# Kernel optimization log

Measured on AMD Instinct MI355X. Metric: run time of the kernel, lower is better.

## Reference

```python
import jax, jax.numpy as jnp
import numpy as np

B, L, V, D = 8, 2048, 1024, 512  # batch, seq (max_len), vocab_size (input feat), embedding_dim

def setup_inputs() -> dict:
    key = jax.random.key(0)
    kx, kq, kk, kv = jax.random.split(key, 4)
    scale = 1.0 / np.sqrt(V)
    return {
        "x": jax.random.normal(kx, (B, L, V), dtype=jnp.float32),
        "Wq": jax.random.uniform(kq, (D, V), dtype=jnp.float32, minval=-scale, maxval=scale),
        "Wk": jax.random.uniform(kk, (D, V), dtype=jnp.float32, minval=-scale, maxval=scale),
        "Wv": jax.random.uniform(kv, (D, V), dtype=jnp.float32, minval=-scale, maxval=scale),
    }

def reference(x, Wq, Wk, Wv):
    # nn.Linear without bias: y = x @ W.T
    q = jnp.einsum('blv,dv->bld', x, Wq)
    k = jnp.einsum('blv,dv->bld', x, Wk)
    v = jnp.einsum('blv,dv->bld', x, Wv)
    scores = jnp.einsum('bqd,bkd->bqk', q, k) / jnp.sqrt(jnp.float32(D))
    attn = jax.nn.softmax(scores, axis=2)
    return jnp.einsum('bqk,bkd->bqd', attn, v)
```

## Files before the change

### kernel.cpp

```cpp
#include <hip/hip_runtime.h>
#include <cstdint>
#include <cstddef>


typedef __attribute__((ext_vector_type(8))) __bf16 bf16x8;
typedef __attribute__((ext_vector_type(4))) float f32x4;
typedef __attribute__((ext_vector_type(4))) unsigned short ushort4v;
typedef __attribute__((ext_vector_type(4))) unsigned int uint4v;

__device__ __forceinline__ unsigned short f2bf(float f) {
  unsigned u = __float_as_uint(f);
  return (unsigned short)((u + 0x7fffu + ((u >> 16) & 1u)) >> 16);
}

__device__ __forceinline__ void async_load16(const unsigned short* g, unsigned short* l) {
  __builtin_amdgcn_global_load_lds(
      (__attribute__((address_space(1))) void*)(g),
      (__attribute__((address_space(3))) void*)(l), 16, 0, 0);
}

__global__ __launch_bounds__(256) void cvt_f32_bf16(const float* __restrict__ src,
                                                    unsigned short* __restrict__ dst) {
  int i = (blockIdx.x * 256 + threadIdx.x) * 4;
  float4 v = *(const float4*)(src + i);
  ushort4v o;
  o.x = f2bf(v.x); o.y = f2bf(v.y); o.z = f2bf(v.z); o.w = f2bf(v.w);
  *(ushort4v*)(dst + i) = o;
}

__global__ __launch_bounds__(256) void cvt_w3(const float* __restrict__ a,
                                              const float* __restrict__ b,
                                              const float* __restrict__ c,
                                              unsigned short* __restrict__ dst) {
  int bx = blockIdx.x;
  const float* src = (bx < 512) ? a : (bx < 1024) ? b : c;
  int seg = (bx < 512) ? 0 : (bx < 1024) ? 1 : 2;
  int i = ((bx & 511) * 256 + threadIdx.x) * 4;
  float4 v = *(const float4*)(src + i);
  ushort4v o;
  o.x = f2bf(v.x); o.y = f2bf(v.y); o.z = f2bf(v.z); o.w = f2bf(v.w);
  *(ushort4v*)(dst + seg * 524288 + i) = o;
}

__device__ __forceinline__ void stage_tile(
    const unsigned short* __restrict__ A, const unsigned short* __restrict__ B,
    size_t ldA, size_t ldB, unsigned short* buf, int tid, int k0) {
  int r = tid >> 3, c = tid & 7;
  int cs = (c ^ (r & 7)) * 8;
  #pragma unroll
  for (int p = 0; p < 4; ++p)
    async_load16(&A[(size_t)(p * 64 + r) * ldA + k0 + cs], &buf[(p * 512 + tid) * 8]);
  unsigned short* bb = buf + 16384;
  #pragma unroll
  for (int p = 0; p < 2; ++p)
    async_load16(&B[(size_t)(p * 64 + r) * ldB + k0 + cs], &bb[(p * 512 + tid) * 8]);
}

template <int NT, bool RSUM>
__device__ __forceinline__ void gemm_core(
    const unsigned short* __restrict__ A, const unsigned short* __restrict__ B,
    size_t ldA, size_t ldB, unsigned short* smem, int tid,
    f32x4 (&acc)[4][4], float (&rsum)[4]) {
  const int lane = tid & 63;
  const int wid = tid >> 6;
  const int wm = wid & 3, wn = wid >> 2;
  const int cl = lane & 15, g = lane >> 4;

  stage_tile(A, B, ldA, ldB, smem + 0 * 24576, tid, 0);
  stage_tile(A, B, ldA, ldB, smem + 1 * 24576, tid, 64);

  int cur = 0;
  for (int t = 0; t < NT; ++t) {
    if (t == NT - 1) asm volatile("s_waitcnt vmcnt(0)" ::: "memory");
    else             asm volatile("s_waitcnt vmcnt(6)" ::: "memory");
    __builtin_amdgcn_s_barrier();
    if (t + 2 < NT) {
      int nb = cur + 2; if (nb >= 3) nb -= 3;
      stage_tile(A, B, ldA, ldB, smem + nb * 24576, tid, (t + 2) * 64);
    }
    const unsigned short* sA = smem + cur * 24576;
    const unsigned short* sB = sA + 16384;

    bf16x8 aF[4][2], bF[4][2];
    #pragma unroll
    for (int mt = 0; mt < 4; ++mt)
      #pragma unroll
      for (int kh = 0; kh < 2; ++kh) {
        int row = wm * 64 + mt * 16 + cl;
        int ch = (kh * 4 + g) ^ (row & 7);
        aF[mt][kh] = *(const bf16x8*)&sA[(row * 8 + ch) * 8];
      }
    #pragma unroll
    for (int nt = 0; nt < 4; ++nt)
      #pragma unroll
      for (int kh = 0; kh < 2; ++kh) {
        int row = wn * 64 + nt * 16 + cl;
        int ch = (kh * 4 + g) ^ (row & 7);
        bF[nt][kh] = *(const bf16x8*)&sB[(row * 8 + ch) * 8];
      }

    if (RSUM) {
      #pragma unroll
      for (int mt = 0; mt < 4; ++mt)
        #pragma unroll
        for (int kh = 0; kh < 2; ++kh) {
          uint4v u = __builtin_bit_cast(uint4v, aF[mt][kh]);
          #pragma unroll
          for (int q = 0; q < 4; ++q)
            rsum[mt] += __uint_as_float(u[q] << 16) +
                        __uint_as_float(u[q] & 0xffff0000u);
        }
    }

    __builtin_amdgcn_s_setprio(1);
    #pragma unroll
    for (int mt = 0; mt < 4; ++mt)
      #pragma unroll
      for (int nt = 0; nt < 4; ++nt)
        #pragma unroll
        for (int kh = 0; kh < 2; ++kh)
          acc[mt][nt] = __builtin_amdgcn_mfma_f32_16x16x32_bf16(
              aF[mt][kh], bF[nt][kh], acc[mt][nt], 0, 0, 0);
    __builtin_amdgcn_s_setprio(0);

    cur = (cur == 2) ? 0 : cur + 1;
  }
}

__global__ __launch_bounds__(512, 2) void gemm_qkv(
    const unsigned short* __restrict__ A0,
    const unsigned short* __restrict__ Bw,
    unsigned short* __restrict__ qk,
    unsigned short* __restrict__ vT) {
  extern __shared__ __align__(16) unsigned short smem[];
  const int tid = threadIdx.x;
  const unsigned short* A = A0 + (size_t)blockIdx.y * 256 * 1024;
  const unsigned short* B = Bw + (size_t)blockIdx.x * 128 * 1024;

  f32x4 acc[4][4] = {};
  float rsum[4];
  gemm_core<16, false>(A, B, 1024, 1024, smem, tid, acc, rsum);

  const int lane = tid & 63, wid = tid >> 6;
  const int wm = wid & 3, wn = wid >> 2, cl = lane & 15, g = lane >> 4;

  if (blockIdx.x < 8) {
    unsigned short* Cc = qk + (size_t)blockIdx.y * 256 * 1024 + (size_t)blockIdx.x * 128;
    #pragma unroll
    for (int mt = 0; mt < 4; ++mt)
      #pragma unroll
      for (int nt = 0; nt < 4; ++nt) {
        int col = wn * 64 + nt * 16 + cl;
        int row0 = wm * 64 + mt * 16 + g * 4;
        #pragma unroll
        for (int j = 0; j < 4; ++j)
          Cc[(size_t)(row0 + j) * 1024 + col] = f2bf(acc[mt][nt][j]);
      }
  } else {
    int nvx = blockIdx.x - 8;
    #pragma unroll
    for (int mt = 0; mt < 4; ++mt)
      #pragma unroll
      for (int nt = 0; nt < 4; ++nt) {
        int d = nvx * 128 + wn * 64 + nt * 16 + cl;
        int grow0 = blockIdx.y * 256 + wm * 64 + mt * 16 + g * 4;
        int b = grow0 >> 11, l0 = grow0 & 2047;
        ushort4v o;
        o.x = f2bf(acc[mt][nt][0]); o.y = f2bf(acc[mt][nt][1]);
        o.z = f2bf(acc[mt][nt][2]); o.w = f2bf(acc[mt][nt][3]);
        *(ushort4v*)&vT[(size_t)b * 1048576 + (size_t)d * 2048 + l0] = o;
      }
  }
}

__global__ __launch_bounds__(512, 2) void gemm_exp(
    const unsigned short* __restrict__ qk,
    unsigned short* __restrict__ S, float scale) {
  extern __shared__ __align__(16) unsigned short smem[];
  const int tid = threadIdx.x;
  const unsigned short* A  = qk + (size_t)blockIdx.z * 2097152 + (size_t)blockIdx.y * 256 * 1024;
  const unsigned short* Bk = qk + 512 + (size_t)blockIdx.z * 2097152 + (size_t)blockIdx.x * 128 * 1024;

  f32x4 acc[4][4] = {};
  float rsum[4];
  gemm_core<8, false>(A, Bk, 1024, 1024, smem, tid, acc, rsum);

  const int lane = tid & 63, wid = tid >> 6;
  const int wm = wid & 3, wn = wid >> 2, cl = lane & 15, g = lane >> 4;

  unsigned short* Cc = S + (size_t)blockIdx.z * 4194304 +
                       (size_t)blockIdx.y * 256 * 2048 + (size_t)blockIdx.x * 128;
  #pragma unroll
  for (int mt = 0; mt < 4; ++mt)
    #pragma unroll
    for (int nt = 0; nt < 4; ++nt) {
      int col = wn * 64 + nt * 16 + cl;
      int row0 = wm * 64 + mt * 16 + g * 4;
      #pragma unroll
      for (int j = 0; j < 4; ++j)
        Cc[(size_t)(row0 + j) * 2048 + col] =
            f2bf(__expf(acc[mt][nt][j] * scale));
    }
}

__global__ __launch_bounds__(512, 2) void gemm_pv(
    const unsigned short* __restrict__ P, const unsigned short* __restrict__ vT,
    float* __restrict__ out) {
  extern __shared__ __align__(16) unsigned short smem[];
  const int tid = threadIdx.x;
  const int b = blockIdx.z;
  const int m0 = blockIdx.y * 256, n0 = blockIdx.x * 128;
  const unsigned short* A  = P + (size_t)b * 4194304 + (size_t)m0 * 2048;
  const unsigned short* Bv = vT + (size_t)b * 1048576 + (size_t)n0 * 2048;

  f32x4 acc[4][4] = {};
  float rsum[4] = {0.f, 0.f, 0.f, 0.f};
  gemm_core<32, true>(A, Bv, 2048, 2048, smem, tid, acc, rsum);

  const int lane = tid & 63, wid = tid >> 6;
  const int wm = wid & 3, wn = wid >> 2, cl = lane & 15, g = lane >> 4;

  float* rs = (float*)(smem + 73728);
  #pragma unroll
  for (int mt = 0; mt < 4; ++mt) {
    float v = rsum[mt];
    v += __shfl_xor(v, 16, 64);
    v += __shfl_xor(v, 32, 64);
    if (wn == 0 && lane < 16) rs[wm * 64 + mt * 16 + lane] = v;
  }
  __syncthreads();

  #pragma unroll
  for (int mt = 0; mt < 4; ++mt) {
    int row0l = wm * 64 + mt * 16 + g * 4;
    float inv[4];
    #pragma unroll
    for (int j = 0; j < 4; ++j) inv[j] = __builtin_amdgcn_rcpf(rs[row0l + j]);
    #pragma unroll
    for (int nt = 0; nt < 4; ++nt) {
      int col = n0 + wn * 64 + nt * 16 + cl;
      float* op = out + ((size_t)b * 2048 + m0 + row0l) * 512 + col;
      #pragma unroll
      for (int j = 0; j < 4; ++j)
        op[(size_t)j * 512] = acc[mt][nt][j] * inv[j];
    }
  }
}

extern "C" void kernel_launch(void* const* d_in, const int* in_sizes, int n_in,
                              void* d_out, int out_size, void* d_ws, size_t ws_size,
                              hipStream_t stream) {
  const float* x  = (const float*)d_in[0];
  const float* Wq = (const float*)d_in[1];
  const float* Wk = (const float*)d_in[2];
  const float* Wv = (const float*)d_in[3];
  float* out = (float*)d_out;
  char* ws = (char*)d_ws;

  unsigned short* xb = (unsigned short*)ws;
  unsigned short* S  = (unsigned short*)ws;
  unsigned short* wf = (unsigned short*)(ws + 33554432);
  unsigned short* qk = (unsigned short*)(ws + 67108864);
  unsigned short* vT = (unsigned short*)(ws + 100663296);

  const float rsqrtD = 0.044194173824159216f;

  static bool inited = false;
  if (!inited) {
    hipFuncSetAttribute((const void*)gemm_qkv,
                        hipFuncAttributeMaxDynamicSharedMemorySize, 148480);
    hipFuncSetAttribute((const void*)gemm_exp,
                        hipFuncAttributeMaxDynamicSharedMemorySize, 148480);
    hipFuncSetAttribute((const void*)gemm_pv,
                        hipFuncAttributeMaxDynamicSharedMemorySize, 148480);
    inited = true;
  }

  hipLaunchKernelGGL(cvt_f32_bf16, dim3(16384), dim3(256), 0, stream, x, xb);
  hipLaunchKernelGGL(cvt_w3, dim3(1536), dim3(256), 0, stream, Wq, Wk, Wv, wf);

  hipLaunchKernelGGL(gemm_qkv, dim3(12, 64, 1), dim3(512), 147456, stream,
                     xb, wf, qk, vT);

  hipLaunchKernelGGL(gemm_exp, dim3(16, 8, 8), dim3(512), 147456, stream,
                     qk, S, rsqrtD);

  hipLaunchKernelGGL(gemm_pv, dim3(4, 8, 8), dim3(512), 148480, stream,
                     S, vT, out);

  (void)in_sizes; (void)n_in; (void)out_size; (void)ws_size;
}
```

Measured before the change: 269.1 us.

## Remap warps to 2x4 grid and split each k-step into two barrier-synced halves

Changes the warp layout from 4x2 (64x64 per warp) to 2x4 (128x32 per warp), so each warp loads fewer B fragments. Each k-iteration now runs as two phases over the top and bottom A halves, and the async global-to-LDS staging of the next tile is interleaved between them. Explicit lgkmcnt/vmcnt waits and extra barriers are added. The aim is to overlap LDS reads and global prefetch with MFMA work, at the cost of more barriers per iteration and more LDS reads of A.

New measurement: 302.5 us. +12.4%, slower.

```diff
diff --git a/kernel.cpp b/kernel.cpp
--- a/kernel.cpp
+++ b/kernel.cpp
@@ -42,63 +42,79 @@
   *(ushort4v*)(dst + seg * 524288 + i) = o;
 }
 
-__device__ __forceinline__ void stage_tile(
-    const unsigned short* __restrict__ A, const unsigned short* __restrict__ B,
-    size_t ldA, size_t ldB, unsigned short* buf, int tid, int k0) {
+__device__ __forceinline__ void stage_Ahalf(const unsigned short* __restrict__ A,
+                                            size_t ldA, unsigned short* buf,
+                                            int tid, int k0, int h) {
   int r = tid >> 3, c = tid & 7;
   int cs = (c ^ (r & 7)) * 8;
   #pragma unroll
-  for (int p = 0; p < 4; ++p)
-    async_load16(&A[(size_t)(p * 64 + r) * ldA + k0 + cs], &buf[(p * 512 + tid) * 8]);
-  unsigned short* bb = buf + 16384;
-  #pragma unroll
   for (int p = 0; p < 2; ++p)
-    async_load16(&B[(size_t)(p * 64 + r) * ldB + k0 + cs], &bb[(p * 512 + tid) * 8]);
+    async_load16(&A[(size_t)(h * 128 + p * 64 + r) * ldA + k0 + cs],
+                 &buf[(h * 1024 + p * 512 + tid) * 8]);
+}
+
+__device__ __forceinline__ void stage_B(const unsigned short* __restrict__ B,
+                                        size_t ldB, unsigned short* buf,
+                                        int tid, int k0) {
+  int r = tid >> 3, c = tid & 7;
+  int cs = (c ^ (r & 7)) * 8;
+  #pragma unroll
+  for (int p = 0; p < 2; ++p)
+    async_load16(&B[(size_t)(p * 64 + r) * ldB + k0 + cs],
+                 &buf[16384 + (p * 512 + tid) * 8]);
 }
 
 template <int NT, bool RSUM>
 __device__ __forceinline__ void gemm_core(
     const unsigned short* __restrict__ A, const unsigned short* __restrict__ B,
     size_t ldA, size_t ldB, unsigned short* smem, int tid,
-    f32x4 (&acc)[4][4], float (&rsum)[4]) {
-  const int lane = tid & 63;
-  const int wid = tid >> 6;
-  const int wm = wid & 3, wn = wid >> 2;
+    f32x4 (&acc)[8][2], float (&rsum)[8]) {
+  const int lane = tid & 63, wid = tid >> 6;
+  const int wm = wid & 1, wn = wid >> 1;
   const int cl = lane & 15, g = lane >> 4;
 
-  stage_tile(A, B, ldA, ldB, smem + 0 * 24576, tid, 0);
-  stage_tile(A, B, ldA, ldB, smem + 1 * 24576, tid, 64);
+  stage_Ahalf(A, ldA, smem, tid, 0, 0);
+  stage_Ahalf(A, ldA, smem, tid, 0, 1);
+  stage_B(B, ldB, smem, tid, 0);
+  stage_Ahalf(A, ldA, smem + 24576, tid, 64, 0);
+  stage_Ahalf(A, ldA, smem + 24576, tid, 64, 1);
+  stage_B(B, ldB, smem + 24576, tid, 64);
+  asm volatile("s_waitcnt vmcnt(6)" ::: "memory");
+  __builtin_amdgcn_s_barrier();
 
   int cur = 0;
   for (int t = 0; t < NT; ++t) {
-    if (t == NT - 1) asm volatile("s_waitcnt vmcnt(0)" ::: "memory");
-    else             asm volatile("s_waitcnt vmcnt(6)" ::: "memory");
-    __builtin_amdgcn_s_barrier();
-    if (t + 2 < NT) {
-      int nb = cur + 2; if (nb >= 3) nb -= 3;
-      stage_tile(A, B, ldA, ldB, smem + nb * 24576, tid, (t + 2) * 64);
-    }
     const unsigned short* sA = smem + cur * 24576;
     const unsigned short* sB = sA + 16384;
-
-    bf16x8 aF[4][2], bF[4][2];
+    int nb = cur + 2; if (nb >= 3) nb -= 3;
+    unsigned short* nbuf = smem + nb * 24576;
+    const bool doStage = (t + 2 < NT);
+    const int k2 = (t + 2) * 64;
+
+    bf16x8 aF[4][2], bF[2][2];
+
     #pragma unroll
     for (int mt = 0; mt < 4; ++mt)
       #pragma unroll
       for (int kh = 0; kh < 2; ++kh) {
-        int row = wm * 64 + mt * 16 + cl;
-        int ch = (kh * 4 + g) ^ (row & 7);
-        aF[mt][kh] = *(const bf16x8*)&sA[(row * 8 + ch) * 8];
-      }
-    #pragma unroll
-    for (int nt = 0; nt < 4; ++nt)
+        int rr = wm * 128 + mt * 16 + cl;
+        aF[mt][kh] = *(const bf16x8*)&sA[(rr * 8 + ((kh * 4 + g) ^ (rr & 7))) * 8];
+      }
+    #pragma unroll
+    for (int nt = 0; nt < 2; ++nt)
       #pragma unroll
       for (int kh = 0; kh < 2; ++kh) {
-        int row = wn * 64 + nt * 16 + cl;
-        int ch = (kh * 4 + g) ^ (row & 7);
-        bF[nt][kh] = *(const bf16x8*)&sB[(row * 8 + ch) * 8];
-      }
-
+        int rb = wn * 32 + nt * 16 + cl;
+        bF[nt][kh] = *(const bf16x8*)&sB[(rb * 8 + ((kh * 4 + g) ^ (rb & 7))) * 8];
+      }
+    if (doStage) {
+      stage_Ahalf(A, ldA, nbuf, tid, k2, 0);
+      stage_Ahalf(A, ldA, nbuf, tid, k2, 1);
+    }
+    asm volatile("s_waitcnt lgkmcnt(8)" ::: "memory");
+    __builtin_amdgcn_s_barrier();
+    asm volatile("s_waitcnt lgkmcnt(0)" ::: "memory");
+    __builtin_amdgcn_sched_barrier(0);
     if (RSUM) {
       #pragma unroll
       for (int mt = 0; mt < 4; ++mt)
@@ -111,19 +127,59 @@
                         __uint_as_float(u[q] & 0xffff0000u);
         }
     }
-
     __builtin_amdgcn_s_setprio(1);
     #pragma unroll
     for (int mt = 0; mt < 4; ++mt)
       #pragma unroll
-      for (int nt = 0; nt < 4; ++nt)
+      for (int nt = 0; nt < 2; ++nt)
         #pragma unroll
         for (int kh = 0; kh < 2; ++kh)
           acc[mt][nt] = __builtin_amdgcn_mfma_f32_16x16x32_bf16(
               aF[mt][kh], bF[nt][kh], acc[mt][nt], 0, 0, 0);
     __builtin_amdgcn_s_setprio(0);
-
-    cur = (cur == 2) ? 0 : cur + 1;
+    __builtin_amdgcn_s_barrier();
+
+    #pragma unroll
+    for (int mt = 0; mt < 4; ++mt)
+      #pragma unroll
+      for (int kh = 0; kh < 2; ++kh) {
+        int rr = wm * 128 + (mt + 4) * 16 + cl;
+        aF[mt][kh] = *(const bf16x8*)&sA[(rr * 8 + ((kh * 4 + g) ^ (rr & 7))) * 8];
+      }
+    if (doStage) {
+      stage_B(B, ldB, nbuf, tid, k2);
+      asm volatile("s_waitcnt vmcnt(6)" ::: "memory");
+    } else {
+      asm volatile("s_waitcnt vmcnt(0)" ::: "memory");
+    }
+    __builtin_amdgcn_s_barrier();
+    asm volatile("s_waitcnt lgkmcnt(0)" ::: "memory");
+    __builtin_amdgcn_sched_barrier(0);
+    if (RSUM) {
+      #pragma unroll
+      for (int mt = 0; mt < 4; ++mt)
+        #pragma unroll
+        for (int kh = 0; kh < 2; ++kh) {
+          uint4v u = __builtin_bit_cast(uint4v, aF[mt][kh]);
+          #pragma unroll
+          for (int q = 0; q < 4; ++q)
+            rsum[mt + 4] += __uint_as_float(u[q] << 16) +
+                            __uint_as_float(u[q] & 0xffff0000u);
+        }
+    }
+    __builtin_amdgcn_s_setprio(1);
+    #pragma unroll
+    for (int mt = 0; mt < 4; ++mt)
+      #pragma unroll
+      for (int nt = 0; nt < 2; ++nt)
+        #pragma unroll
+        for (int kh = 0; kh < 2; ++kh)
+          acc[mt + 4][nt] = __builtin_amdgcn_mfma_f32_16x16x32_bf16(
+              aF[mt][kh], bF[nt][kh], acc[mt + 4][nt], 0, 0, 0);
+    __builtin_amdgcn_s_setprio(0);
+    __builtin_amdgcn_s_barrier();
+
+    cur = cur + 1; if (cur == 3) cur = 0;
   }
 }
 
@@ -137,21 +193,21 @@
   const unsigned short* A = A0 + (size_t)blockIdx.y * 256 * 1024;
   const unsigned short* B = Bw + (size_t)blockIdx.x * 128 * 1024;
 
-  f32x4 acc[4][4] = {};
-  float rsum[4];
+  f32x4 acc[8][2] = {};
+  float rsum[8];
   gemm_core<16, false>(A, B, 1024, 1024, smem, tid, acc, rsum);
 
   const int lane = tid & 63, wid = tid >> 6;
-  const int wm = wid & 3, wn = wid >> 2, cl = lane & 15, g = lane >> 4;
+  const int wm = wid & 1, wn = wid >> 1, cl = lane & 15, g = lane >> 4;
 
   if (blockIdx.x < 8) {
     unsigned short* Cc = qk + (size_t)blockIdx.y * 256 * 1024 + (size_t)blockIdx.x * 128;
     #pragma unroll
-    for (int mt = 0; mt < 4; ++mt)
-      #pragma unroll
-      for (int nt = 0; nt < 4; ++nt) {
-        int col = wn * 64 + nt * 16 + cl;
-        int row0 = wm * 64 + mt * 16 + g * 4;
+    for (int mt = 0; mt < 8; ++mt)
+      #pragma unroll
+      for (int nt = 0; nt < 2; ++nt) {
+        int col = wn * 32 + nt * 16 + cl;
+        int row0 = wm * 128 + mt * 16 + g * 4;
         #pragma unroll
         for (int j = 0; j < 4; ++j)
           Cc[(size_t)(row0 + j) * 1024 + col] = f2bf(acc[mt][nt][j]);
@@ -159,11 +215,11 @@
   } else {
     int nvx = blockIdx.x - 8;
     #pragma unroll
-    for (int mt = 0; mt < 4; ++mt)
-      #pragma unroll
-      for (int nt = 0; nt < 4; ++nt) {
-        int d = nvx * 128 + wn * 64 + nt * 16 + cl;
-        int grow0 = blockIdx.y * 256 + wm * 64 + mt * 16 + g * 4;
+    for (int mt = 0; mt < 8; ++mt)
+      #pragma unroll
+      for (int nt = 0; nt < 2; ++nt) {
+        int d = nvx * 128 + wn * 32 + nt * 16 + cl;
+        int grow0 = blockIdx.y * 256 + wm * 128 + mt * 16 + g * 4;
         int b = grow0 >> 11, l0 = grow0 & 2047;
         ushort4v o;
         o.x = f2bf(acc[mt][nt][0]); o.y = f2bf(acc[mt][nt][1]);
@@ -181,21 +237,21 @@
   const unsigned short* A  = qk + (size_t)blockIdx.z * 2097152 + (size_t)blockIdx.y * 256 * 1024;
   const unsigned short* Bk = qk + 512 + (size_t)blockIdx.z * 2097152 + (size_t)blockIdx.x * 128 * 1024;
 
-  f32x4 acc[4][4] = {};
-  float rsum[4];
+  f32x4 acc[8][2] = {};
+  float rsum[8];
   gemm_core<8, false>(A, Bk, 1024, 1024, smem, tid, acc, rsum);
 
   const int lane = tid & 63, wid = tid >> 6;
-  const int wm = wid & 3, wn = wid >> 2, cl = lane & 15, g = lane >> 4;
+  const int wm = wid & 1, wn = wid >> 1, cl = lane & 15, g = lane >> 4;
 
   unsigned short* Cc = S + (size_t)blockIdx.z * 4194304 +
                        (size_t)blockIdx.y * 256 * 2048 + (size_t)blockIdx.x * 128;
   #pragma unroll
-  for (int mt = 0; mt < 4; ++mt)
-    #pragma unroll
-    for (int nt = 0; nt < 4; ++nt) {
-      int col = wn * 64 + nt * 16 + cl;
-      int row0 = wm * 64 + mt * 16 + g * 4;
+  for (int mt = 0; mt < 8; ++mt)
+    #pragma unroll
+    for (int nt = 0; nt < 2; ++nt) {
+      int col = wn * 32 + nt * 16 + cl;
+      int row0 = wm * 128 + mt * 16 + g * 4;
       #pragma unroll
       for (int j = 0; j < 4; ++j)
         Cc[(size_t)(row0 + j) * 2048 + col] =
@@ -213,32 +269,32 @@
   const unsigned short* A  = P + (size_t)b * 4194304 + (size_t)m0 * 2048;
   const unsigned short* Bv = vT + (size_t)b * 1048576 + (size_t)n0 * 2048;
 
-  f32x4 acc[4][4] = {};
-  float rsum[4] = {0.f, 0.f, 0.f, 0.f};
+  f32x4 acc[8][2] = {};
+  float rsum[8] = {};
   gemm_core<32, true>(A, Bv, 2048, 2048, smem, tid, acc, rsum);
 
   const int lane = tid & 63, wid = tid >> 6;
-  const int wm = wid & 3, wn = wid >> 2, cl = lane & 15, g = lane >> 4;
+  const int wm = wid & 1, wn = wid >> 1, cl = lane & 15, g = lane >> 4;
 
   float* rs = (float*)(smem + 73728);
   #pragma unroll
-  for (int mt = 0; mt < 4; ++mt) {
+  for (int mt = 0; mt < 8; ++mt) {
     float v = rsum[mt];
     v += __shfl_xor(v, 16, 64);
     v += __shfl_xor(v, 32, 64);
-    if (wn == 0 && lane < 16) rs[wm * 64 + mt * 16 + lane] = v;
+    if (wn == 0 && lane < 16) rs[wm * 128 + mt * 16 + lane] = v;
   }
   __syncthreads();
 
   #pragma unroll
-  for (int mt = 0; mt < 4; ++mt) {
-    int row0l = wm * 64 + mt * 16 + g * 4;
+  for (int mt = 0; mt < 8; ++mt) {
+    int row0l = wm * 128 + mt * 16 + g * 4;
     float inv[4];
     #pragma unroll
     for (int j = 0; j < 4; ++j) inv[j] = __builtin_amdgcn_rcpf(rs[row0l + j]);
     #pragma unroll
-    for (int nt = 0; nt < 4; ++nt) {
-      int col = n0 + wn * 64 + nt * 16 + cl;
+    for (int nt = 0; nt < 2; ++nt) {
+      int col = n0 + wn * 32 + nt * 16 + cl;
       float* op = out + ((size_t)b * 2048 + m0 + row0l) * 512 + col;
       #pragma unroll
       for (int j = 0; j < 4; ++j)
```

## Replace triple-buffered 256x128 GEMMs with single-buffer 128x128 tiles and swizzled block order

Applied to the files above, without the earlier changes.

All three GEMM kernels drop the shared triple-buffered pipelined core and use a simple 128x128 tile on 256 threads with a single LDS buffer, synchronised by two barriers per k-step. Block indices are remapped so that neighbouring blocks share the same batch or row panel, which is meant to improve L2 reuse. The smaller tiles and static shared memory should allow more blocks per CU. In exchange, the async loads are no longer overlapped with MFMA work, and each tile gets less operand reuse.

Result: faster. 262.3 us (-2.5%).

```diff
diff --git a/kernel.cpp b/kernel.cpp
--- a/kernel.cpp
+++ b/kernel.cpp
@@ -42,110 +42,62 @@
   *(ushort4v*)(dst + seg * 524288 + i) = o;
 }
 
-__device__ __forceinline__ void stage_tile(
-    const unsigned short* __restrict__ A, const unsigned short* __restrict__ B,
-    size_t ldA, size_t ldB, unsigned short* buf, int tid, int k0) {
-  int r = tid >> 3, c = tid & 7;
-  int cs = (c ^ (r & 7)) * 8;
-  #pragma unroll
-  for (int p = 0; p < 4; ++p)
-    async_load16(&A[(size_t)(p * 64 + r) * ldA + k0 + cs], &buf[(p * 512 + tid) * 8]);
-  unsigned short* bb = buf + 16384;
-  #pragma unroll
-  for (int p = 0; p < 2; ++p)
-    async_load16(&B[(size_t)(p * 64 + r) * ldB + k0 + cs], &bb[(p * 512 + tid) * 8]);
-}
-
-template <int NT, bool RSUM>
-__device__ __forceinline__ void gemm_core(
-    const unsigned short* __restrict__ A, const unsigned short* __restrict__ B,
-    size_t ldA, size_t ldB, unsigned short* smem, int tid,
-    f32x4 (&acc)[4][4], float (&rsum)[4]) {
-  const int lane = tid & 63;
-  const int wid = tid >> 6;
-  const int wm = wid & 3, wn = wid >> 2;
-  const int cl = lane & 15, g = lane >> 4;
-
-  stage_tile(A, B, ldA, ldB, smem + 0 * 24576, tid, 0);
-  stage_tile(A, B, ldA, ldB, smem + 1 * 24576, tid, 64);
-
-  int cur = 0;
-  for (int t = 0; t < NT; ++t) {
-    if (t == NT - 1) asm volatile("s_waitcnt vmcnt(0)" ::: "memory");
-    else             asm volatile("s_waitcnt vmcnt(6)" ::: "memory");
-    __builtin_amdgcn_s_barrier();
-    if (t + 2 < NT) {
-      int nb = cur + 2; if (nb >= 3) nb -= 3;
-      stage_tile(A, B, ldA, ldB, smem + nb * 24576, tid, (t + 2) * 64);
-    }
-    const unsigned short* sA = smem + cur * 24576;
-    const unsigned short* sB = sA + 16384;
-
-    bf16x8 aF[4][2], bF[4][2];
-    #pragma unroll
-    for (int mt = 0; mt < 4; ++mt)
-      #pragma unroll
-      for (int kh = 0; kh < 2; ++kh) {
-        int row = wm * 64 + mt * 16 + cl;
-        int ch = (kh * 4 + g) ^ (row & 7);
-        aF[mt][kh] = *(const bf16x8*)&sA[(row * 8 + ch) * 8];
-      }
-    #pragma unroll
-    for (int nt = 0; nt < 4; ++nt)
-      #pragma unroll
-      for (int kh = 0; kh < 2; ++kh) {
-        int row = wn * 64 + nt * 16 + cl;
-        int ch = (kh * 4 + g) ^ (row & 7);
-        bF[nt][kh] = *(const bf16x8*)&sB[(row * 8 + ch) * 8];
-      }
-
-    if (RSUM) {
-      #pragma unroll
-      for (int mt = 0; mt < 4; ++mt)
-        #pragma unroll
-        for (int kh = 0; kh < 2; ++kh) {
-          uint4v u = __builtin_bit_cast(uint4v, aF[mt][kh]);
-          #pragma unroll
-          for (int q = 0; q < 4; ++q)
-            rsum[mt] += __uint_as_float(u[q] << 16) +
-                        __uint_as_float(u[q] & 0xffff0000u);
-        }
-    }
-
-    __builtin_amdgcn_s_setprio(1);
-    #pragma unroll
-    for (int mt = 0; mt < 4; ++mt)
-      #pragma unroll
-      for (int nt = 0; nt < 4; ++nt)
-        #pragma unroll
-        for (int kh = 0; kh < 2; ++kh)
-          acc[mt][nt] = __builtin_amdgcn_mfma_f32_16x16x32_bf16(
-              aF[mt][kh], bF[nt][kh], acc[mt][nt], 0, 0, 0);
-    __builtin_amdgcn_s_setprio(0);
-
-    cur = (cur == 2) ? 0 : cur + 1;
-  }
-}
-
-__global__ __launch_bounds__(512, 2) void gemm_qkv(
+
+__global__ __launch_bounds__(256) void gemm_qkv(
     const unsigned short* __restrict__ A0,
     const unsigned short* __restrict__ Bw,
     unsigned short* __restrict__ qk,
     unsigned short* __restrict__ vT) {
-  extern __shared__ __align__(16) unsigned short smem[];
+  __shared__ unsigned short sA[128 * 64];
+  __shared__ unsigned short sB[128 * 64];
   const int tid = threadIdx.x;
-  const unsigned short* A = A0 + (size_t)blockIdx.y * 256 * 1024;
-  const unsigned short* B = Bw + (size_t)blockIdx.x * 128 * 1024;
+  const int lane = tid & 63, wid = tid >> 6;
+  const int wm = wid & 1, wn = wid >> 1;
+  const int cl = lane & 15, g = lane >> 4;
+
+  int flat = blockIdx.x + blockIdx.y * 12;
+  int sub = flat >> 3;
+  int bxp = sub % 12;
+  int byp = (flat & 7) * 16 + sub / 12;
+
+  const unsigned short* A = A0 + (size_t)byp * 128 * 1024;
+  const unsigned short* B = Bw + (size_t)bxp * 128 * 1024;
 
   f32x4 acc[4][4] = {};
-  float rsum[4];
-  gemm_core<16, false>(A, B, 1024, 1024, smem, tid, acc, rsum);
-
-  const int lane = tid & 63, wid = tid >> 6;
-  const int wm = wid & 3, wn = wid >> 2, cl = lane & 15, g = lane >> 4;
-
-  if (blockIdx.x < 8) {
-    unsigned short* Cc = qk + (size_t)blockIdx.y * 256 * 1024 + (size_t)blockIdx.x * 128;
+
+  for (int k0 = 0; k0 < 1024; k0 += 64) {
+    __syncthreads();
+    #pragma unroll
+    for (int p = 0; p < 4; ++p) {
+      int u = p * 256 + tid;
+      int r = u >> 3, cs = (u & 7) ^ (r & 7);
+      async_load16(&A[(size_t)r * 1024 + k0 + cs * 8], &sA[u * 8]);
+      async_load16(&B[(size_t)r * 1024 + k0 + cs * 8], &sB[u * 8]);
+    }
+    __syncthreads();
+
+    bf16x8 aF[4][2], bF[4][2];
+    #pragma unroll
+    for (int t = 0; t < 4; ++t)
+      #pragma unroll
+      for (int kh = 0; kh < 2; ++kh) {
+        int ra = wm * 64 + t * 16 + cl;
+        aF[t][kh] = *(const bf16x8*)&sA[(ra * 8 + ((kh * 4 + g) ^ (ra & 7))) * 8];
+        int rb = wn * 64 + t * 16 + cl;
+        bF[t][kh] = *(const bf16x8*)&sB[(rb * 8 + ((kh * 4 + g) ^ (rb & 7))) * 8];
+      }
+    #pragma unroll
+    for (int mt = 0; mt < 4; ++mt)
+      #pragma unroll
+      for (int nt = 0; nt < 4; ++nt)
+        #pragma unroll
+        for (int kh = 0; kh < 2; ++kh)
+          acc[mt][nt] = __builtin_amdgcn_mfma_f32_16x16x32_bf16(
+              aF[mt][kh], bF[nt][kh], acc[mt][nt], 0, 0, 0);
+  }
+
+  if (bxp < 8) {
+    unsigned short* Cc = qk + (size_t)byp * 128 * 1024 + (size_t)bxp * 128;
     #pragma unroll
     for (int mt = 0; mt < 4; ++mt)
       #pragma unroll
@@ -157,13 +109,13 @@
           Cc[(size_t)(row0 + j) * 1024 + col] = f2bf(acc[mt][nt][j]);
       }
   } else {
-    int nvx = blockIdx.x - 8;
+    int nvx = bxp - 8;
     #pragma unroll
     for (int mt = 0; mt < 4; ++mt)
       #pragma unroll
       for (int nt = 0; nt < 4; ++nt) {
         int d = nvx * 128 + wn * 64 + nt * 16 + cl;
-        int grow0 = blockIdx.y * 256 + wm * 64 + mt * 16 + g * 4;
+        int grow0 = byp * 128 + wm * 64 + mt * 16 + g * 4;
         int b = grow0 >> 11, l0 = grow0 & 2047;
         ushort4v o;
         o.x = f2bf(acc[mt][nt][0]); o.y = f2bf(acc[mt][nt][1]);
@@ -173,23 +125,58 @@
   }
 }
 
-__global__ __launch_bounds__(512, 2) void gemm_exp(
+__global__ __launch_bounds__(256) void gemm_exp(
     const unsigned short* __restrict__ qk,
     unsigned short* __restrict__ S, float scale) {
-  extern __shared__ __align__(16) unsigned short smem[];
+  __shared__ unsigned short sA[128 * 64];
+  __shared__ unsigned short sB[128 * 64];
   const int tid = threadIdx.x;
-  const unsigned short* A  = qk + (size_t)blockIdx.z * 2097152 + (size_t)blockIdx.y * 256 * 1024;
-  const unsigned short* Bk = qk + 512 + (size_t)blockIdx.z * 2097152 + (size_t)blockIdx.x * 128 * 1024;
+  const int lane = tid & 63, wid = tid >> 6;
+  const int wm = wid & 1, wn = wid >> 1;
+  const int cl = lane & 15, g = lane >> 4;
+
+  int flat = blockIdx.x + (blockIdx.y << 4) + (blockIdx.z << 8);
+  int z = flat & 7, rem = flat >> 3;
+  int bxp = rem & 15, byp = rem >> 4;
+
+  const unsigned short* A  = qk + (size_t)z * 2097152 + (size_t)byp * 128 * 1024;
+  const unsigned short* Bk = qk + 512 + (size_t)z * 2097152 + (size_t)bxp * 128 * 1024;
 
   f32x4 acc[4][4] = {};
-  float rsum[4];
-  gemm_core<8, false>(A, Bk, 1024, 1024, smem, tid, acc, rsum);
-
-  const int lane = tid & 63, wid = tid >> 6;
-  const int wm = wid & 3, wn = wid >> 2, cl = lane & 15, g = lane >> 4;
-
-  unsigned short* Cc = S + (size_t)blockIdx.z * 4194304 +
-                       (size_t)blockIdx.y * 256 * 2048 + (size_t)blockIdx.x * 128;
+
+  for (int k0 = 0; k0 < 512; k0 += 64) {
+    __syncthreads();
+    #pragma unroll
+    for (int p = 0; p < 4; ++p) {
+      int u = p * 256 + tid;
+      int r = u >> 3, cs = (u & 7) ^ (r & 7);
+      async_load16(&A[(size_t)r * 1024 + k0 + cs * 8], &sA[u * 8]);
+      async_load16(&Bk[(size_t)r * 1024 + k0 + cs * 8], &sB[u * 8]);
+    }
+    __syncthreads();
+
+    bf16x8 aF[4][2], bF[4][2];
+    #pragma unroll
+    for (int t = 0; t < 4; ++t)
+      #pragma unroll
+      for (int kh = 0; kh < 2; ++kh) {
+        int ra = wm * 64 + t * 16 + cl;
+        aF[t][kh] = *(const bf16x8*)&sA[(ra * 8 + ((kh * 4 + g) ^ (ra & 7))) * 8];
+        int rb = wn * 64 + t * 16 + cl;
+        bF[t][kh] = *(const bf16x8*)&sB[(rb * 8 + ((kh * 4 + g) ^ (rb & 7))) * 8];
+      }
+    #pragma unroll
+    for (int mt = 0; mt < 4; ++mt)
+      #pragma unroll
+      for (int nt = 0; nt < 4; ++nt)
+        #pragma unroll
+        for (int kh = 0; kh < 2; ++kh)
+          acc[mt][nt] = __builtin_amdgcn_mfma_f32_16x16x32_bf16(
+              aF[mt][kh], bF[nt][kh], acc[mt][nt], 0, 0, 0);
+  }
+
+  unsigned short* Cc = S + (size_t)z * 4194304 +
+                       (size_t)byp * 128 * 2048 + (size_t)bxp * 128;
   #pragma unroll
   for (int mt = 0; mt < 4; ++mt)
     #pragma unroll
@@ -203,24 +190,69 @@
     }
 }
 
-__global__ __launch_bounds__(512, 2) void gemm_pv(
+__global__ __launch_bounds__(256) void gemm_pv(
     const unsigned short* __restrict__ P, const unsigned short* __restrict__ vT,
     float* __restrict__ out) {
-  extern __shared__ __align__(16) unsigned short smem[];
+  __shared__ unsigned short sA[128 * 64];
+  __shared__ unsigned short sB[128 * 64];
+  __shared__ float rs[128];
   const int tid = threadIdx.x;
-  const int b = blockIdx.z;
-  const int m0 = blockIdx.y * 256, n0 = blockIdx.x * 128;
-  const unsigned short* A  = P + (size_t)b * 4194304 + (size_t)m0 * 2048;
-  const unsigned short* Bv = vT + (size_t)b * 1048576 + (size_t)n0 * 2048;
+  const int lane = tid & 63, wid = tid >> 6;
+  const int wm = wid & 1, wn = wid >> 1;
+  const int cl = lane & 15, g = lane >> 4;
+
+  int flat = blockIdx.x + (blockIdx.y << 2) + (blockIdx.z << 6);
+  int z = flat & 7, rem = flat >> 3;
+  int bxp = rem & 3, byp = rem >> 2;
+
+  const int m0 = byp * 128, n0 = bxp * 128;
+  const unsigned short* A  = P + (size_t)z * 4194304 + (size_t)m0 * 2048;
+  const unsigned short* Bv = vT + (size_t)z * 1048576 + (size_t)n0 * 2048;
 
   f32x4 acc[4][4] = {};
   float rsum[4] = {0.f, 0.f, 0.f, 0.f};
-  gemm_core<32, true>(A, Bv, 2048, 2048, smem, tid, acc, rsum);
-
-  const int lane = tid & 63, wid = tid >> 6;
-  const int wm = wid & 3, wn = wid >> 2, cl = lane & 15, g = lane >> 4;
-
-  float* rs = (float*)(smem + 73728);
+
+  for (int k0 = 0; k0 < 2048; k0 += 64) {
+    __syncthreads();
+    #pragma unroll
+    for (int p = 0; p < 4; ++p) {
+      int u = p * 256 + tid;
+      int r = u >> 3, cs = (u & 7) ^ (r & 7);
+      async_load16(&A[(size_t)r * 2048 + k0 + cs * 8], &sA[u * 8]);
+      async_load16(&Bv[(size_t)r * 2048 + k0 + cs * 8], &sB[u * 8]);
+    }
+    __syncthreads();
+
+    bf16x8 aF[4][2], bF[4][2];
+    #pragma unroll
+    for (int t = 0; t < 4; ++t)
+      #pragma unroll
+      for (int kh = 0; kh < 2; ++kh) {
+        int ra = wm * 64 + t * 16 + cl;
+        aF[t][kh] = *(const bf16x8*)&sA[(ra * 8 + ((kh * 4 + g) ^ (ra & 7))) * 8];
+        int rb = wn * 64 + t * 16 + cl;
+        bF[t][kh] = *(const bf16x8*)&sB[(rb * 8 + ((kh * 4 + g) ^ (rb & 7))) * 8];
+      }
+    #pragma unroll
+    for (int t = 0; t < 4; ++t)
+      #pragma unroll
+      for (int kh = 0; kh < 2; ++kh) {
+        uint4v u = __builtin_bit_cast(uint4v, aF[t][kh]);
+        #pragma unroll
+        for (int q = 0; q < 4; ++q)
+          rsum[t] += __uint_as_float(u[q] << 16) +
+                     __uint_as_float(u[q] & 0xffff0000u);
+      }
+    #pragma unroll
+    for (int mt = 0; mt < 4; ++mt)
+      #pragma unroll
+      for (int nt = 0; nt < 4; ++nt)
+        #pragma unroll
+        for (int kh = 0; kh < 2; ++kh)
+          acc[mt][nt] = __builtin_amdgcn_mfma_f32_16x16x32_bf16(
+              aF[mt][kh], bF[nt][kh], acc[mt][nt], 0, 0, 0);
+  }
+
   #pragma unroll
   for (int mt = 0; mt < 4; ++mt) {
     float v = rsum[mt];
@@ -239,7 +271,7 @@
     #pragma unroll
     for (int nt = 0; nt < 4; ++nt) {
       int col = n0 + wn * 64 + nt * 16 + cl;
-      float* op = out + ((size_t)b * 2048 + m0 + row0l) * 512 + col;
+      float* op = out + ((size_t)z * 2048 + m0 + row0l) * 512 + col;
       #pragma unroll
       for (int j = 0; j < 4; ++j)
         op[(size_t)j * 512] = acc[mt][nt][j] * inv[j];
@@ -265,28 +297,14 @@
 
   const float rsqrtD = 0.044194173824159216f;
 
-  static bool inited = false;
-  if (!inited) {
-    hipFuncSetAttribute((const void*)gemm_qkv,
-                        hipFuncAttributeMaxDynamicSharedMemorySize, 148480);
-    hipFuncSetAttribute((const void*)gemm_exp,
-                        hipFuncAttributeMaxDynamicSharedMemorySize, 148480);
-    hipFuncSetAttribute((const void*)gemm_pv,
-                        hipFuncAttributeMaxDynamicSharedMemorySize, 148480);
-    inited = true;
-  }
-
   hipLaunchKernelGGL(cvt_f32_bf16, dim3(16384), dim3(256), 0, stream, x, xb);
   hipLaunchKernelGGL(cvt_w3, dim3(1536), dim3(256), 0, stream, Wq, Wk, Wv, wf);
 
-  hipLaunchKernelGGL(gemm_qkv, dim3(12, 64, 1), dim3(512), 147456, stream,
-                     xb, wf, qk, vT);
-
-  hipLaunchKernelGGL(gemm_exp, dim3(16, 8, 8), dim3(512), 147456, stream,
-                     qk, S, rsqrtD);
-
-  hipLaunchKernelGGL(gemm_pv, dim3(4, 8, 8), dim3(512), 148480, stream,
-                     S, vT, out);
+  hipLaunchKernelGGL(gemm_qkv, dim3(12, 128, 1), dim3(256), 0, stream, xb, wf, qk, vT);
+
+  hipLaunchKernelGGL(gemm_exp, dim3(16, 16, 8), dim3(256), 0, stream, qk, S, rsqrtD);
+
+  hipLaunchKernelGGL(gemm_pv, dim3(4, 16, 8), dim3(256), 0, stream, S, vT, out);
 
   (void)in_sizes; (void)n_in; (void)out_size; (void)ws_size;
 }
```
